# Optimization experiments

Hardware: AMD Instinct MI355X
Metric: run time of the kernel (lower is better)

The kernel has to match this reference:

```python
import jax, jax.numpy as jnp
import numpy as np

DIM = 128
HEADS = 8
RBF_K = 16
N_LIG = 20000
N_PROT = 80000
E = 262144
HEAD_DIM = DIM // HEADS
SCALE = HEAD_DIM ** -0.5


def setup_inputs() -> dict:
    key = jax.random.key(0)
    ks = jax.random.split(key, 16)
    inp = {
        "ligand_x": jax.random.normal(ks[0], (N_LIG, DIM), dtype=jnp.float32),
        "protein_x": jax.random.normal(ks[1], (N_PROT, DIM), dtype=jnp.float32),
        "cross_edges": jax.random.randint(ks[2], (E, 2), 0, N_LIG, dtype=jnp.int64)
        if jax.config.jax_enable_x64 else jax.random.randint(ks[2], (E, 2), 0, N_LIG, dtype=jnp.int32),
        "cross_attr": jax.random.uniform(ks[3], (E, RBF_K), dtype=jnp.float32),
        "Wq": jax.random.normal(ks[4], (DIM, DIM), dtype=jnp.float32) * (DIM ** -0.5),
        "bq": jax.random.normal(ks[5], (DIM,), dtype=jnp.float32) * 0.02,
        "Wk": jax.random.normal(ks[6], (DIM, DIM), dtype=jnp.float32) * (DIM ** -0.5),
        "bk": jax.random.normal(ks[7], (DIM,), dtype=jnp.float32) * 0.02,
        "Wv": jax.random.normal(ks[8], (DIM, DIM), dtype=jnp.float32) * (DIM ** -0.5),
        "bv": jax.random.normal(ks[9], (DIM,), dtype=jnp.float32) * 0.02,
        "Wo": jax.random.normal(ks[10], (DIM, DIM), dtype=jnp.float32) * (DIM ** -0.5),
        "bo": jax.random.normal(ks[11], (DIM,), dtype=jnp.float32) * 0.02,
        "Wr": jax.random.normal(ks[12], (RBF_K, HEADS), dtype=jnp.float32) * (RBF_K ** -0.5),
        "br": jax.random.normal(ks[13], (HEADS,), dtype=jnp.float32) * 0.02,
        "lig_start": 0,
        "prot_start": 0,
    }
    return inp


def _heads(t):
    return t.reshape(t.shape[0], HEADS, HEAD_DIM)


def _cross_attend(q_nodes, k_nodes, v_nodes, dst_idx, src_idx, rbf_bias, n_dst):
    # gather per-edge q/k/v: [E, H, D]
    qe = q_nodes[dst_idx]
    ke = k_nodes[src_idx]
    ve = v_nodes[src_idx]
    logits = jnp.einsum("ehd,ehd->eh", qe, ke) * SCALE + rbf_bias  # [E, H]
    # segment softmax over edges grouped by destination node
    m = jax.ops.segment_max(logits, dst_idx, num_segments=n_dst)  # [N, H]
    ex = jnp.exp(logits - m[dst_idx])
    s = jax.ops.segment_sum(ex, dst_idx, num_segments=n_dst)  # [N, H]
    w = ex / (s[dst_idx] + 1e-8)  # [E, H]
    agg = jax.ops.segment_sum(w[:, :, None] * ve, dst_idx, num_segments=n_dst)
    return agg.reshape(n_dst, HEADS * HEAD_DIM)


def reference(ligand_x, protein_x, cross_edges, cross_attr, Wq, bq, Wk, bk, Wv, bv,
              Wo, bo, Wr, br, lig_start, prot_start):
    n_lig, n_prot = ligand_x.shape[0], protein_x.shape[0]
    q_l = _heads(ligand_x @ Wq + bq)
    k_p = _heads(protein_x @ Wk + bk)
    v_p = _heads(protein_x @ Wv + bv)
    q_p = _heads(protein_x @ Wq + bq)
    k_l = _heads(ligand_x @ Wk + bk)
    v_l = _heads(ligand_x @ Wv + bv)

    lig_local = cross_edges[:, 0] - lig_start
    prot_local = cross_edges[:, 1] - prot_start
    rbf_bias = cross_attr @ Wr + br  # [E, heads]

    lig_agg = _cross_attend(q_l, k_p, v_p, lig_local, prot_local, rbf_bias, n_lig)
    prot_agg = _cross_attend(q_p, k_l, v_l, prot_local, lig_local, rbf_bias, n_prot)

    ligand_out = lig_agg @ Wo + bo   # dropout is identity at inference
    protein_out = prot_agg @ Wo + bo
    return (ligand_out, protein_out)
```

## Files before the change

kernel.cpp:

```cpp
#include <hip/hip_runtime.h>
#include <hip/hip_bf16.h>

typedef unsigned short u16;
typedef __attribute__((ext_vector_type(8))) short short8;
typedef __attribute__((ext_vector_type(4))) float f32x4;

__device__ __forceinline__ float bf2f(u16 u){
  union { unsigned int i; float f; } c; c.i = ((unsigned int)u) << 16; return c.f;
}
__device__ __forceinline__ u16 f2bf(float f){
  union { float f; unsigned int i; } c; c.f = f;
  unsigned int x = c.i;
  return (u16)((x + 0x7FFFu + ((x >> 16) & 1u)) >> 16);
}

__device__ __forceinline__ int edge_get(const int* __restrict__ e32, int i64, int e, int c){
  int idx = 2 * e + c;
  return i64 ? e32[2 * idx] : e32[idx];
}

__global__ void detect_kernel(const u16* __restrict__ lig16,
                              const int* __restrict__ e32, int* __restrict__ flags)
{
  int lane = threadIdx.x;
  int cnt = 0, nz = 0;
  #pragma unroll
  for (int j = 0; j < 4; j++){
    u16 u = lig16[(lane * 4 + j) * 2];
    int ex = (u >> 7) & 0xFF;
    if (ex >= 96 && ex < 160) cnt++;
    if (e32[(lane * 4 + j) * 2 + 1] != 0) nz++;
  }
  #pragma unroll
  for (int off = 1; off < 64; off <<= 1){
    cnt += __shfl_xor(cnt, off);
    nz  += __shfl_xor(nz, off);
  }
  if (lane == 0){
    flags[0] = (cnt < 128) ? 1 : 0;
    flags[1] = (nz == 0) ? 1 : 0;
  }
}

__global__ __launch_bounds__(256) void prep_w(
    const void* __restrict__ Wq, const void* __restrict__ Wk,
    const void* __restrict__ Wv, const void* __restrict__ Wo,
    const void* __restrict__ bq, const void* __restrict__ bk,
    const void* __restrict__ bv, const void* __restrict__ bo,
    u16* __restrict__ Wt, float* __restrict__ biasP, const int* __restrict__ flags)
{
  int mat = blockIdx.x, tid = threadIdx.x;
  const void* W = (mat == 0) ? Wq : (mat == 1) ? Wk : (mat == 2) ? Wv : Wo;
  const void* b = (mat == 0) ? bq : (mat == 1) ? bk : (mat == 2) ? bv : bo;
  int F = flags[0];
  u16* dst = Wt + mat * 16384;
  #pragma unroll 4
  for (int j = 0; j < 64; j++){
    int idx = tid + j * 256;
    u16 w = F ? f2bf(((const float*)W)[idx]) : ((const u16*)W)[idx];
    dst[(idx & 127) * 128 + (idx >> 7)] = w;
  }
  if (tid < 128)
    biasP[mat * 128 + tid] = F ? ((const float*)b)[tid] : bf2f(((const u16*)b)[tid]);
}

__global__ __launch_bounds__(256) void gemm_multi(
    const void* __restrict__ A0, int M0, const void* __restrict__ A1, int M1, int mb0,
    const u16* __restrict__ Wt, const float* __restrict__ biasP, int wbase, int nm,
    u16* __restrict__ O0b, u16* __restrict__ O1b, u16* __restrict__ O2b,
    float* __restrict__ O0f,
    int a_force_bf16, int final_out, const int* __restrict__ flags)
{
  __shared__ __align__(16) char smem[52224];
  u16 (*As)[136]  = (u16(*)[136])smem;
  u16 (*Ws)[136]  = (u16(*)[136])(smem + 17408);
  float (*Fs)[132] = (float(*)[132])(smem + 17408);

  int tid = threadIdx.x;
  int F = flags[0];
  int AF = a_force_bf16 ? 0 : F;
  int xb = blockIdx.x;
  const void* A; int M, m0, orow;
  if (xb < mb0){ A = A0; M = M0; m0 = xb * 64;          orow = m0; }
  else         { A = A1; M = M1; m0 = (xb - mb0) * 64;  orow = M0 + m0; }

  if (AF){
    const float* Af = (const float*)A;
    #pragma unroll
    for (int j = 0; j < 8; j++){
      int idx = tid + j * 256;
      int m = idx >> 5, k4 = idx & 31;
      float4 v = make_float4(0.f, 0.f, 0.f, 0.f);
      if (m0 + m < M) v = *(const float4*)&Af[(size_t)(m0 + m) * 128 + k4 * 4];
      ushort4 o; o.x = f2bf(v.x); o.y = f2bf(v.y); o.z = f2bf(v.z); o.w = f2bf(v.w);
      *(ushort4*)&As[m][k4 * 4] = o;
    }
  } else {
    const u16* Au = (const u16*)A;
    #pragma unroll
    for (int j = 0; j < 8; j++){
      int idx = tid + j * 256;
      int m = idx >> 5, k4 = idx & 31;
      ushort4 v = make_ushort4(0, 0, 0, 0);
      if (m0 + m < M) v = *(const ushort4*)&Au[(size_t)(m0 + m) * 128 + k4 * 4];
      *(ushort4*)&As[m][k4 * 4] = v;
    }
  }
  {
    const u16* Wsrc = Wt + (size_t)wbase * 16384;
    #pragma unroll
    for (int j = 0; j < 8; j++){
      int idx = tid + j * 256;
      *(short8*)&Ws[idx >> 4][(idx & 15) * 8] = *(const short8*)&Wsrc[idx * 8];
    }
  }
  __syncthreads();

  int wave = tid >> 6, lane = tid & 63;
  int quad = lane >> 4, ml = lane & 15;

  short8 af[4];
  #pragma unroll
  for (int kk = 0; kk < 4; kk++)
    af[kk] = *(const short8*)&As[wave * 16 + ml][kk * 32 + quad * 8];

  int f32out = final_out && F;

  for (int mat = 0; mat < nm; mat++){
    f32x4 acc[8];
    #pragma unroll
    for (int nt = 0; nt < 8; nt++) acc[nt] = (f32x4){0.f, 0.f, 0.f, 0.f};

    #pragma unroll
    for (int nt = 0; nt < 8; nt++){
      #pragma unroll
      for (int kk = 0; kk < 4; kk++){
        short8 bfr = *(const short8*)&Ws[nt * 16 + ml][kk * 32 + quad * 8];
        acc[nt] = __builtin_amdgcn_mfma_f32_16x16x32_bf16(af[kk], bfr, acc[nt], 0, 0, 0);
      }
    }

    __syncthreads();
    const float* bp = biasP + (size_t)(wbase + mat) * 128;
    #pragma unroll
    for (int nt = 0; nt < 8; nt++){
      float bcol = bp[nt * 16 + ml];
      #pragma unroll
      for (int r = 0; r < 4; r++)
        Fs[wave * 16 + quad * 4 + r][nt * 16 + ml] = acc[nt][r] + bcol;
    }
    __syncthreads();

    if (f32out){
      #pragma unroll
      for (int j = 0; j < 8; j++){
        int u = tid + j * 256;
        int row = u >> 5, c4 = (u & 31) * 4;
        if (m0 + row < M)
          *(float4*)&O0f[(size_t)(orow + row) * 128 + c4] = *(const float4*)&Fs[row][c4];
      }
    } else {
      u16* Cb = (mat == 0) ? O0b : ((mat == 1) ? O1b : O2b);
      #pragma unroll
      for (int j = 0; j < 4; j++){
        int u = tid + j * 256;
        int row = u >> 4, c8 = (u & 15) * 8;
        if (m0 + row < M){
          float4 x = *(const float4*)&Fs[row][c8];
          float4 y = *(const float4*)&Fs[row][c8 + 4];
          short8 s8;
          s8[0] = (short)f2bf(x.x); s8[1] = (short)f2bf(x.y);
          s8[2] = (short)f2bf(x.z); s8[3] = (short)f2bf(x.w);
          s8[4] = (short)f2bf(y.x); s8[5] = (short)f2bf(y.y);
          s8[6] = (short)f2bf(y.z); s8[7] = (short)f2bf(y.w);
          *(short8*)&Cb[(size_t)(orow + row) * 128 + c8] = s8;
        }
      }
    }

    if (mat + 1 < nm){
      __syncthreads();
      const u16* Wsrc = Wt + (size_t)(wbase + mat + 1) * 16384;
      #pragma unroll
      for (int j = 0; j < 8; j++){
        int idx = tid + j * 256;
        *(short8*)&Ws[idx >> 4][(idx & 15) * 8] = *(const short8*)&Wsrc[idx * 8];
      }
      __syncthreads();
    }
  }
}

__global__ __launch_bounds__(256) void edge_pre(
    const void* __restrict__ attr, const void* __restrict__ Wr,
    const void* __restrict__ br, float* __restrict__ ebias,
    const int* __restrict__ edges, const int* __restrict__ ls_p,
    const int* __restrict__ ps_p, int* __restrict__ cnt, int nlig, int E_,
    const int* __restrict__ flags)
{
  __shared__ float w[16][8];
  __shared__ float b[8];
  int tid = threadIdx.x;
  int F = flags[0];
  if (tid < 128) w[tid >> 3][tid & 7] = F ? ((const float*)Wr)[tid] : bf2f(((const u16*)Wr)[tid]);
  if (tid < 8)   b[tid] = F ? ((const float*)br)[tid] : bf2f(((const u16*)br)[tid]);
  __syncthreads();
  int e = blockIdx.x * 256 + tid;
  if (e >= E_) return;

  int I64 = flags[1];
  int dl = edge_get(edges, I64, e, 0) - ls_p[0];
  int dp = edge_get(edges, I64, e, 1) - ps_p[0];
  atomicAdd(&cnt[dl], 1);
  atomicAdd(&cnt[nlig + dp], 1);

  float a[16];
  if (F){
    const float* af = (const float*)attr;
    #pragma unroll
    for (int j = 0; j < 4; j++){
      float4 t = *(const float4*)&af[e * 16 + j * 4];
      a[4*j] = t.x; a[4*j+1] = t.y; a[4*j+2] = t.z; a[4*j+3] = t.w;
    }
  } else {
    const u16* au = (const u16*)attr;
    #pragma unroll
    for (int j = 0; j < 4; j++){
      ushort4 t = *(const ushort4*)&au[e * 16 + j * 4];
      a[4*j] = bf2f(t.x); a[4*j+1] = bf2f(t.y); a[4*j+2] = bf2f(t.z); a[4*j+3] = bf2f(t.w);
    }
  }
  #pragma unroll
  for (int hh = 0; hh < 8; hh++){
    float s = b[hh];
    #pragma unroll
    for (int r = 0; r < 16; r++) s += a[r] * w[r][hh];
    ebias[e * 8 + hh] = s;
  }
}

__global__ __launch_bounds__(256) void scan_blocksum(
    const int* __restrict__ cnt, int* __restrict__ bsum, int n)
{
  __shared__ int red[4];
  int tid = threadIdx.x;
  int i = blockIdx.x * 256 + tid;
  int v = (i < n) ? cnt[i] : 0;
  #pragma unroll
  for (int off = 1; off < 64; off <<= 1) v += __shfl_xor(v, off);
  if ((tid & 63) == 0) red[tid >> 6] = v;
  __syncthreads();
  if (tid == 0) bsum[blockIdx.x] = red[0] + red[1] + red[2] + red[3];
}

__global__ __launch_bounds__(512) void scan_bsum(
    int* __restrict__ bsum, int* __restrict__ boff, int nb)
{
  __shared__ int buf[512];
  int tid = threadIdx.x;
  int v = (tid < nb) ? bsum[tid] : 0;
  buf[tid] = v; __syncthreads();
  for (int off = 1; off < 512; off <<= 1){
    int t = (tid >= off) ? buf[tid - off] : 0;
    __syncthreads();
    buf[tid] += t;
    __syncthreads();
  }
  if (tid < nb) boff[tid] = buf[tid] - v;
}

__global__ __launch_bounds__(256) void scan_final(
    const int* __restrict__ cnt, const int* __restrict__ boff,
    int* __restrict__ offs, int* __restrict__ cursor, int n)
{
  __shared__ int buf[256];
  int tid = threadIdx.x;
  int i = blockIdx.x * 256 + tid;
  int v = (i < n) ? cnt[i] : 0;
  buf[tid] = v; __syncthreads();
  for (int off = 1; off < 256; off <<= 1){
    int t = (tid >= off) ? buf[tid - off] : 0;
    __syncthreads();
    buf[tid] += t;
    __syncthreads();
  }
  int excl = buf[tid] - v + boff[blockIdx.x];
  if (i < n){
    offs[i] = excl;
    cursor[i] = excl;
    if (i == n - 1) offs[n] = excl + v;
  }
}

__global__ __launch_bounds__(256) void scatter_kernel(
    const int* __restrict__ edges, const int* __restrict__ ls_p,
    const int* __restrict__ ps_p, int* __restrict__ cursor,
    int2* __restrict__ sorted, int nlig, int E_,
    const int* __restrict__ flags)
{
  int e = blockIdx.x * 256 + threadIdx.x;
  if (e >= E_) return;
  int I64 = flags[1];
  int dl = edge_get(edges, I64, e, 0) - ls_p[0];
  int dp = edge_get(edges, I64, e, 1) - ps_p[0];
  int p1 = atomicAdd(&cursor[dl], 1);        sorted[p1] = make_int2(e, nlig + dp);
  int p2 = atomicAdd(&cursor[nlig + dp], 1); sorted[p2] = make_int2(e, dl);
}

__global__ __launch_bounds__(256) void attn_kernel(
    const u16* __restrict__ Q, const u16* __restrict__ K, const u16* __restrict__ V,
    const int2* __restrict__ sorted, const int* __restrict__ offs,
    const float* __restrict__ ebias, u16* __restrict__ AGG, int ntot)
{
  int t = blockIdx.x * 4 + (threadIdx.x >> 6);
  if (t >= ntot) return;
  int lane = threadIdx.x & 63, h = lane >> 3;

  ushort2 qu = *(const ushort2*)&Q[(size_t)t * 128 + lane * 2];
  float q0 = bf2f(qu.x), q1 = bf2f(qu.y);

  int beg = offs[t], end = offs[t + 1];
  float m = -INFINITY, l = 0.f, a0 = 0.f, a1 = 0.f;

  int2 nxt = make_int2(0, 0);
  if (beg < end) nxt = sorted[beg];
  for (int i = beg; i < end; i++){
    int2 cur = nxt;
    if (i + 1 < end) nxt = sorted[i + 1];
    int src = cur.y;
    ushort2 ku = *(const ushort2*)&K[(size_t)src * 128 + lane * 2];
    ushort2 vu = *(const ushort2*)&V[(size_t)src * 128 + lane * 2];
    float eb = ebias[(size_t)cur.x * 8 + h];
    float part = q0 * bf2f(ku.x) + q1 * bf2f(ku.y);
    part += __shfl_xor(part, 1);
    part += __shfl_xor(part, 2);
    part += __shfl_xor(part, 4);
    float logit = part * 0.25f + eb;
    float nm = fmaxf(m, logit);
    float alpha = __expf(m - nm);
    float p = __expf(logit - nm);
    a0 = a0 * alpha + p * bf2f(vu.x);
    a1 = a1 * alpha + p * bf2f(vu.y);
    l = l * alpha + p;
    m = nm;
  }
  float inv = 1.f / (l + 1e-8f);
  ushort2 o; o.x = f2bf(a0 * inv); o.y = f2bf(a1 * inv);
  *(ushort2*)&AGG[(size_t)t * 128 + lane * 2] = o;
}

extern "C" void kernel_launch(void* const* d_in, const int* in_sizes, int n_in,
                              void* d_out, int out_size, void* d_ws, size_t ws_size,
                              hipStream_t stream)
{
  const void* ligand_x  = d_in[0];
  const void* protein_x = d_in[1];
  const int* edges      = (const int*)d_in[2];
  const void* attr      = d_in[3];
  const void* Wq = d_in[4];  const void* bq = d_in[5];
  const void* Wk = d_in[6];  const void* bk = d_in[7];
  const void* Wv = d_in[8];  const void* bv = d_in[9];
  const void* Wo = d_in[10]; const void* bo = d_in[11];
  const void* Wr = d_in[12]; const void* br = d_in[13];
  const int* ls_p = (const int*)d_in[14];
  const int* ps_p = (const int*)d_in[15];

  const int nlig = in_sizes[0] / 128;
  const int nprot = in_sizes[1] / 128;
  const int E = in_sizes[2] / 2;
  const int ntot = nlig + nprot;

  char* w = (char*)d_ws;
  size_t off = 0;
  auto alloc = [&](size_t bytes) -> void* {
    void* p = w + off;
    off = (off + bytes + 255) & ~(size_t)255;
    return p;
  };
  int*   flags = (int*)alloc(256);
  u16*   Wt    = (u16*)alloc(4 * 16384 * 2);
  float* biasP = (float*)alloc(4 * 128 * 4);
  u16* Qb  = (u16*)alloc((size_t)ntot * 128 * 2);
  u16* Kb  = (u16*)alloc((size_t)ntot * 128 * 2);
  u16* Vb  = (u16*)alloc((size_t)ntot * 128 * 2);
  u16* AGG = (u16*)alloc((size_t)ntot * 128 * 2);
  float* ebias = (float*)alloc((size_t)E * 8 * 4);
  int* cnt    = (int*)alloc((size_t)ntot * 4);
  int* offs   = (int*)alloc((size_t)(ntot + 1) * 4);
  int* cursor = (int*)alloc((size_t)ntot * 4);
  int* bsum   = (int*)alloc(512 * 4);
  int* boff   = (int*)alloc(512 * 4);
  int2* sorted = (int2*)alloc((size_t)2 * E * 8);
  (void)ws_size; (void)n_in; (void)out_size;

  const int mb_l = (nlig + 63) / 64;
  const int mb_p = (nprot + 63) / 64;
  const int mb_t = (ntot + 63) / 64;
  const int eb = (E + 255) / 256;
  const int nb = (ntot + 255) / 256;

  hipMemsetAsync(cnt, 0, (size_t)ntot * 4, stream);
  detect_kernel<<<1, 64, 0, stream>>>((const u16*)ligand_x, edges, flags);
  prep_w<<<4, 256, 0, stream>>>(Wq, Wk, Wv, Wo, bq, bk, bv, bo, Wt, biasP, flags);

  gemm_multi<<<mb_l + mb_p, 256, 0, stream>>>(
      ligand_x, nlig, protein_x, nprot, mb_l,
      Wt, biasP, 0, 3,
      Qb, Kb, Vb, nullptr, 0, 0, flags);

  edge_pre<<<eb, 256, 0, stream>>>(attr, Wr, br, ebias, edges, ls_p, ps_p,
                                   cnt, nlig, E, flags);

  scan_blocksum<<<nb, 256, 0, stream>>>(cnt, bsum, ntot);
  scan_bsum<<<1, 512, 0, stream>>>(bsum, boff, nb);
  scan_final<<<nb, 256, 0, stream>>>(cnt, boff, offs, cursor, ntot);
  scatter_kernel<<<eb, 256, 0, stream>>>(edges, ls_p, ps_p, cursor, sorted, nlig, E, flags);

  attn_kernel<<<(ntot + 3) / 4, 256, 0, stream>>>(Qb, Kb, Vb, sorted, offs, ebias, AGG, ntot);

  gemm_multi<<<mb_t, 256, 0, stream>>>(
      AGG, ntot, nullptr, 0, mb_t,
      Wt, biasP, 3, 1,
      (u16*)d_out, nullptr, nullptr, (float*)d_out,
      1, 1, flags);
}
```

Measured before the change: 340.5 us.

## Interleave K/V rows, unroll attention by two, use single-pass decoupled scan

The gemm now writes K and V into one interleaved buffer with a 256-element row stride, so each edge fetches its K and V from the same row. The attention loop is unrolled to process two edges per step with a combined online-softmax update, and edge indices are made wave-uniform with readfirstlane. The three-kernel prefix scan is replaced by a single kernel in which each block publishes its partial sum and spins on the flags of earlier blocks. That spin depends on earlier blocks being scheduled first, and the per-block loop over all previous flags costs more as the block index grows.

```diff
diff --git a/kernel.cpp b/kernel.cpp
--- a/kernel.cpp
+++ b/kernel.cpp
@@ -7,6 +7,12 @@
 
 __device__ __forceinline__ float bf2f(u16 u){
   union { unsigned int i; float f; } c; c.i = ((unsigned int)u) << 16; return c.f;
+}
+__device__ __forceinline__ float lo2f(unsigned u){
+  union { unsigned int i; float f; } c; c.i = u << 16; return c.f;
+}
+__device__ __forceinline__ float hi2f(unsigned u){
+  union { unsigned int i; float f; } c; c.i = u & 0xffff0000u; return c.f;
 }
 __device__ __forceinline__ u16 f2bf(float f){
   union { float f; unsigned int i; } c; c.f = f;
@@ -68,6 +74,7 @@
     const void* __restrict__ A0, int M0, const void* __restrict__ A1, int M1, int mb0,
     const u16* __restrict__ Wt, const float* __restrict__ biasP, int wbase, int nm,
     u16* __restrict__ O0b, u16* __restrict__ O1b, u16* __restrict__ O2b,
+    int s0, int s1, int s2,
     float* __restrict__ O0f,
     int a_force_bf16, int final_out, const int* __restrict__ flags)
 {
@@ -160,7 +167,8 @@
           *(float4*)&O0f[(size_t)(orow + row) * 128 + c4] = *(const float4*)&Fs[row][c4];
       }
     } else {
-      u16* Cb = (mat == 0) ? O0b : ((mat == 1) ? O1b : O2b);
+      u16* Cb    = (mat == 0) ? O0b : ((mat == 1) ? O1b : O2b);
+      int stride = (mat == 0) ? s0  : ((mat == 1) ? s1  : s2);
       #pragma unroll
       for (int j = 0; j < 4; j++){
         int u = tid + j * 256;
@@ -168,12 +176,12 @@
         if (m0 + row < M){
           float4 x = *(const float4*)&Fs[row][c8];
           float4 y = *(const float4*)&Fs[row][c8 + 4];
-          short8 s8;
-          s8[0] = (short)f2bf(x.x); s8[1] = (short)f2bf(x.y);
-          s8[2] = (short)f2bf(x.z); s8[3] = (short)f2bf(x.w);
-          s8[4] = (short)f2bf(y.x); s8[5] = (short)f2bf(y.y);
-          s8[6] = (short)f2bf(y.z); s8[7] = (short)f2bf(y.w);
-          *(short8*)&Cb[(size_t)(orow + row) * 128 + c8] = s8;
+          short8 t8;
+          t8[0] = (short)f2bf(x.x); t8[1] = (short)f2bf(x.y);
+          t8[2] = (short)f2bf(x.z); t8[3] = (short)f2bf(x.w);
+          t8[4] = (short)f2bf(y.x); t8[5] = (short)f2bf(y.y);
+          t8[6] = (short)f2bf(y.z); t8[7] = (short)f2bf(y.w);
+          *(short8*)&Cb[(size_t)(orow + row) * stride + c8] = t8;
         }
       }
     }
@@ -239,52 +247,43 @@
   }
 }
 
-__global__ __launch_bounds__(256) void scan_blocksum(
-    const int* __restrict__ cnt, int* __restrict__ bsum, int n)
-{
-  __shared__ int red[4];
-  int tid = threadIdx.x;
-  int i = blockIdx.x * 256 + tid;
-  int v = (i < n) ? cnt[i] : 0;
-  #pragma unroll
-  for (int off = 1; off < 64; off <<= 1) v += __shfl_xor(v, off);
-  if ((tid & 63) == 0) red[tid >> 6] = v;
-  __syncthreads();
-  if (tid == 0) bsum[blockIdx.x] = red[0] + red[1] + red[2] + red[3];
-}
-
-__global__ __launch_bounds__(512) void scan_bsum(
-    int* __restrict__ bsum, int* __restrict__ boff, int nb)
-{
-  __shared__ int buf[512];
-  int tid = threadIdx.x;
-  int v = (tid < nb) ? bsum[tid] : 0;
-  buf[tid] = v; __syncthreads();
-  for (int off = 1; off < 512; off <<= 1){
-    int t = (tid >= off) ? buf[tid - off] : 0;
-    __syncthreads();
-    buf[tid] += t;
-    __syncthreads();
-  }
-  if (tid < nb) boff[tid] = buf[tid] - v;
-}
-
-__global__ __launch_bounds__(256) void scan_final(
-    const int* __restrict__ cnt, const int* __restrict__ boff,
-    int* __restrict__ offs, int* __restrict__ cursor, int n)
+__global__ __launch_bounds__(256) void scan_one(
+    const int* __restrict__ cnt, int* __restrict__ offs, int* __restrict__ cursor,
+    int n, int* __restrict__ partial, int* __restrict__ flag)
 {
   __shared__ int buf[256];
-  int tid = threadIdx.x;
-  int i = blockIdx.x * 256 + tid;
+  int b = blockIdx.x, tid = threadIdx.x;
+  int i = b * 256 + tid;
   int v = (i < n) ? cnt[i] : 0;
   buf[tid] = v; __syncthreads();
+  #pragma unroll
   for (int off = 1; off < 256; off <<= 1){
     int t = (tid >= off) ? buf[tid - off] : 0;
     __syncthreads();
     buf[tid] += t;
     __syncthreads();
   }
-  int excl = buf[tid] - v + boff[blockIdx.x];
+  int myincl = buf[tid];
+  if (tid == 0){
+    partial[b] = buf[255];
+    __hip_atomic_store(&flag[b], 1, __ATOMIC_RELEASE, __HIP_MEMORY_SCOPE_AGENT);
+  }
+  int acc = 0;
+  for (int j = tid; j < b; j += 256){
+    while (__hip_atomic_load(&flag[j], __ATOMIC_ACQUIRE, __HIP_MEMORY_SCOPE_AGENT) == 0){
+      __builtin_amdgcn_s_sleep(1);
+    }
+    acc += partial[j];
+  }
+  __syncthreads();
+  buf[tid] = acc; __syncthreads();
+  #pragma unroll
+  for (int off = 128; off > 0; off >>= 1){
+    if (tid < off) buf[tid] += buf[tid + off];
+    __syncthreads();
+  }
+  int prev = buf[0];
+  int excl = myincl - v + prev;
   if (i < n){
     offs[i] = excl;
     cursor[i] = excl;
@@ -308,7 +307,7 @@
 }
 
 __global__ __launch_bounds__(256) void attn_kernel(
-    const u16* __restrict__ Q, const u16* __restrict__ K, const u16* __restrict__ V,
+    const u16* __restrict__ Q, const u16* __restrict__ KV,
     const int2* __restrict__ sorted, const int* __restrict__ offs,
     const float* __restrict__ ebias, u16* __restrict__ AGG, int ntot)
 {
@@ -319,29 +318,60 @@
   ushort2 qu = *(const ushort2*)&Q[(size_t)t * 128 + lane * 2];
   float q0 = bf2f(qu.x), q1 = bf2f(qu.y);
 
-  int beg = offs[t], end = offs[t + 1];
+  int ts = __builtin_amdgcn_readfirstlane(t);
+  int beg = offs[ts], end = offs[ts + 1];
   float m = -INFINITY, l = 0.f, a0 = 0.f, a1 = 0.f;
 
-  int2 nxt = make_int2(0, 0);
-  if (beg < end) nxt = sorted[beg];
-  for (int i = beg; i < end; i++){
-    int2 cur = nxt;
-    if (i + 1 < end) nxt = sorted[i + 1];
-    int src = cur.y;
-    ushort2 ku = *(const ushort2*)&K[(size_t)src * 128 + lane * 2];
-    ushort2 vu = *(const ushort2*)&V[(size_t)src * 128 + lane * 2];
-    float eb = ebias[(size_t)cur.x * 8 + h];
-    float part = q0 * bf2f(ku.x) + q1 * bf2f(ku.y);
-    part += __shfl_xor(part, 1);
-    part += __shfl_xor(part, 2);
-    part += __shfl_xor(part, 4);
-    float logit = part * 0.25f + eb;
-    float nm = fmaxf(m, logit);
+  int i = beg;
+  for (; i + 1 < end; i += 2){
+    int2 c0 = sorted[i];
+    int2 c1 = sorted[i + 1];
+    int s0 = __builtin_amdgcn_readfirstlane(c0.y);
+    int s1 = __builtin_amdgcn_readfirstlane(c1.y);
+    int e0 = __builtin_amdgcn_readfirstlane(c0.x);
+    int e1 = __builtin_amdgcn_readfirstlane(c1.x);
+    const u16* r0 = KV + (size_t)s0 * 256 + lane * 2;
+    const u16* r1 = KV + (size_t)s1 * 256 + lane * 2;
+    unsigned k0p = *(const unsigned*)r0;
+    unsigned v0p = *(const unsigned*)(r0 + 128);
+    unsigned k1p = *(const unsigned*)r1;
+    unsigned v1p = *(const unsigned*)(r1 + 128);
+    float eb0 = ebias[(size_t)e0 * 8 + h];
+    float eb1 = ebias[(size_t)e1 * 8 + h];
+
+    float d0 = fmaf(q0, lo2f(k0p), q1 * hi2f(k0p));
+    d0 += __shfl_xor(d0, 1); d0 += __shfl_xor(d0, 2); d0 += __shfl_xor(d0, 4);
+    float d1 = fmaf(q0, lo2f(k1p), q1 * hi2f(k1p));
+    d1 += __shfl_xor(d1, 1); d1 += __shfl_xor(d1, 2); d1 += __shfl_xor(d1, 4);
+
+    float l0 = fmaf(d0, 0.25f, eb0);
+    float l1 = fmaf(d1, 0.25f, eb1);
+    float nm = fmaxf(m, fmaxf(l0, l1));
     float alpha = __expf(m - nm);
-    float p = __expf(logit - nm);
-    a0 = a0 * alpha + p * bf2f(vu.x);
-    a1 = a1 * alpha + p * bf2f(vu.y);
-    l = l * alpha + p;
+    float p0 = __expf(l0 - nm);
+    float p1 = __expf(l1 - nm);
+    a0 = fmaf(a0, alpha, fmaf(p0, lo2f(v0p), p1 * lo2f(v1p)));
+    a1 = fmaf(a1, alpha, fmaf(p0, hi2f(v0p), p1 * hi2f(v1p)));
+    l  = fmaf(l,  alpha, p0 + p1);
+    m = nm;
+  }
+  if (i < end){
+    int2 c = sorted[i];
+    int s0 = __builtin_amdgcn_readfirstlane(c.y);
+    int e0 = __builtin_amdgcn_readfirstlane(c.x);
+    const u16* r0 = KV + (size_t)s0 * 256 + lane * 2;
+    unsigned k0p = *(const unsigned*)r0;
+    unsigned v0p = *(const unsigned*)(r0 + 128);
+    float eb0 = ebias[(size_t)e0 * 8 + h];
+    float d0 = fmaf(q0, lo2f(k0p), q1 * hi2f(k0p));
+    d0 += __shfl_xor(d0, 1); d0 += __shfl_xor(d0, 2); d0 += __shfl_xor(d0, 4);
+    float l0 = fmaf(d0, 0.25f, eb0);
+    float nm = fmaxf(m, l0);
+    float alpha = __expf(m - nm);
+    float p0 = __expf(l0 - nm);
+    a0 = fmaf(a0, alpha, p0 * lo2f(v0p));
+    a1 = fmaf(a1, alpha, p0 * hi2f(v0p));
+    l  = fmaf(l,  alpha, p0);
     m = nm;
   }
   float inv = 1.f / (l + 1e-8f);
@@ -381,15 +411,15 @@
   u16*   Wt    = (u16*)alloc(4 * 16384 * 2);
   float* biasP = (float*)alloc(4 * 128 * 4);
   u16* Qb  = (u16*)alloc((size_t)ntot * 128 * 2);
-  u16* Kb  = (u16*)alloc((size_t)ntot * 128 * 2);
-  u16* Vb  = (u16*)alloc((size_t)ntot * 128 * 2);
+  u16* KV  = (u16*)alloc((size_t)ntot * 256 * 2);
   u16* AGG = (u16*)alloc((size_t)ntot * 128 * 2);
   float* ebias = (float*)alloc((size_t)E * 8 * 4);
-  int* cnt    = (int*)alloc((size_t)ntot * 4);
-  int* offs   = (int*)alloc((size_t)(ntot + 1) * 4);
-  int* cursor = (int*)alloc((size_t)ntot * 4);
-  int* bsum   = (int*)alloc(512 * 4);
-  int* boff   = (int*)alloc(512 * 4);
+  int* cnt  = (int*)alloc((size_t)ntot * 4);
+  int* flag = (int*)alloc(512 * 4);
+  size_t zero_len = (size_t)((char*)flag - (char*)cnt) + 512 * 4;
+  int* offs    = (int*)alloc((size_t)(ntot + 1) * 4);
+  int* cursor  = (int*)alloc((size_t)ntot * 4);
+  int* partial = (int*)alloc(512 * 4);
   int2* sorted = (int2*)alloc((size_t)2 * E * 8);
   (void)ws_size; (void)n_in; (void)out_size;
 
@@ -399,28 +429,27 @@
   const int eb = (E + 255) / 256;
   const int nb = (ntot + 255) / 256;
 
-  hipMemsetAsync(cnt, 0, (size_t)ntot * 4, stream);
+  hipMemsetAsync(cnt, 0, zero_len, stream);
   detect_kernel<<<1, 64, 0, stream>>>((const u16*)ligand_x, edges, flags);
   prep_w<<<4, 256, 0, stream>>>(Wq, Wk, Wv, Wo, bq, bk, bv, bo, Wt, biasP, flags);
 
   gemm_multi<<<mb_l + mb_p, 256, 0, stream>>>(
       ligand_x, nlig, protein_x, nprot, mb_l,
       Wt, biasP, 0, 3,
-      Qb, Kb, Vb, nullptr, 0, 0, flags);
+      Qb, KV, KV + 128, 128, 256, 256,
+      nullptr, 0, 0, flags);
 
   edge_pre<<<eb, 256, 0, stream>>>(attr, Wr, br, ebias, edges, ls_p, ps_p,
                                    cnt, nlig, E, flags);
 
-  scan_blocksum<<<nb, 256, 0, stream>>>(cnt, bsum, ntot);
-  scan_bsum<<<1, 512, 0, stream>>>(bsum, boff, nb);
-  scan_final<<<nb, 256, 0, stream>>>(cnt, boff, offs, cursor, ntot);
+  scan_one<<<nb, 256, 0, stream>>>(cnt, offs, cursor, ntot, partial, flag);
   scatter_kernel<<<eb, 256, 0, stream>>>(edges, ls_p, ps_p, cursor, sorted, nlig, E, flags);
 
-  attn_kernel<<<(ntot + 3) / 4, 256, 0, stream>>>(Qb, Kb, Vb, sorted, offs, ebias, AGG, ntot);
+  attn_kernel<<<(ntot + 3) / 4, 256, 0, stream>>>(Qb, KV, sorted, offs, ebias, AGG, ntot);
 
   gemm_multi<<<mb_t, 256, 0, stream>>>(
       AGG, ntot, nullptr, 0, mb_t,
       Wt, biasP, 3, 1,
-      (u16*)d_out, nullptr, nullptr, (float*)d_out,
-      1, 1, flags);
-}
+      (u16*)d_out, nullptr, nullptr, 128, 128, 128,
+      (float*)d_out, 1, 1, flags);
+}
```

After: 349.9 us. 1.03x slower.
